# Kernel optimization log

Measured on AMD Instinct MI355X. Metric: run time of the kernel, lower is better.

Reference implementation:

```python
import jax, jax.numpy as jnp
import numpy as np

N = 100000
E = 3200000
NEG_SLOPE = 0.2


def setup_inputs() -> dict:
    key = jax.random.key(0)
    ks = jax.random.split(key, 12)
    x = jax.random.normal(ks[0], (N, 4), dtype=jnp.float32)
    edge_index = jax.random.randint(ks[1], (2, E), 0, N, dtype=jnp.int64)
    # GATConv(4, 16, heads=4): lin (no bias), att_src/att_dst [H, C], bias [H*C]
    W1 = jax.random.normal(ks[2], (4, 4 * 16), dtype=jnp.float32) * 0.5
    as1 = jax.random.normal(ks[3], (4, 16), dtype=jnp.float32) * 0.5
    ad1 = jax.random.normal(ks[4], (4, 16), dtype=jnp.float32) * 0.5
    b1 = jnp.zeros((64,), dtype=jnp.float32)
    # GATConv(64, 2, heads=4)
    W2 = jax.random.normal(ks[5], (64, 4 * 2), dtype=jnp.float32) * 0.125
    as2 = jax.random.normal(ks[6], (4, 2), dtype=jnp.float32) * 0.5
    ad2 = jax.random.normal(ks[7], (4, 2), dtype=jnp.float32) * 0.5
    b2 = jnp.zeros((8,), dtype=jnp.float32)
    # out head Linear(8, 1)
    Wout = jax.random.normal(ks[8], (8, 1), dtype=jnp.float32) * 0.35
    bout = jnp.zeros((1,), dtype=jnp.float32)
    return {"x": x, "edge_index": edge_index, "W1": W1, "as1": as1, "ad1": ad1,
            "b1": b1, "W2": W2, "as2": as2, "ad2": ad2, "b2": b2,
            "Wout": Wout, "bout": bout}


def gat_conv(x, ei, W, a_src, a_dst, b, H, C, n):
    # PyG GATConv (concat=True, negative_slope=0.2), self-loops already in ei
    xw = (x @ W).reshape(n, H, C)                      # [N, H, C]
    src, dst = ei[0], ei[1]
    alpha_s = jnp.einsum('nhc,hc->nh', xw, a_src)      # [N, H]
    alpha_d = jnp.einsum('nhc,hc->nh', xw, a_dst)      # [N, H]
    e = jax.nn.leaky_relu(alpha_s[src] + alpha_d[dst], NEG_SLOPE)  # [E, H]
    # segment softmax over incoming edges of each destination node
    m = jax.ops.segment_max(e, dst, num_segments=n)    # [N, H]
    e = jnp.exp(e - m[dst])
    denom = jax.ops.segment_sum(e, dst, num_segments=n)
    alpha = e / (denom[dst] + 1e-16)                   # [E, H]
    msg = xw[src] * alpha[:, :, None]                  # [E, H, C]
    out = jax.ops.segment_sum(msg, dst, num_segments=n)  # [N, H, C]
    return out.reshape(n, H * C) + b


def reference(x, edge_index, W1, as1, ad1, b1, W2, as2, ad2, b2, Wout, bout):
    n = x.shape[0]
    ar = jnp.arange(n, dtype=edge_index.dtype)
    ei = jnp.concatenate([edge_index, jnp.stack([ar, ar])], axis=1)  # add self-loops
    h = jax.nn.elu(gat_conv(x, ei, W1, as1, ad1, b1, 4, 16, n))       # [N, 64]
    h = jax.nn.elu(gat_conv(h, ei, W2, as2, ad2, b2, 4, 2, n))        # [N, 8]
    g = jnp.mean(h, axis=0, keepdims=True)  # global_mean_pool, batch all zeros -> [1, 8]
    return jax.nn.sigmoid(g @ Wout + bout)  # [1, 1]
```

## Files before the change

### kernel.cpp

```cpp
#include <hip/hip_runtime.h>
#include <hip/hip_fp8.h>

#define NEG 0.2f
#define BSZ 224
#define MAXBUK 512
#define NBIN 512
#define CAP 16384

typedef float v2f __attribute__((ext_vector_type(2)));

__device__ __forceinline__ float elufast(float x){ return x > 0.0f ? x : __expf(x) - 1.0f; }
__device__ __forceinline__ float b2f(unsigned short b){ return __uint_as_float((unsigned)b << 16); }
__device__ __forceinline__ unsigned short f2b(float x){
    unsigned u = __float_as_uint(x);
    return (unsigned short)((u + 0x7FFFu + ((u >> 16) & 1u)) >> 16);
}

__device__ __forceinline__ void fma8(uint2 r, float w, v2f* acc){
    v2f w2 = {w, w};
    v2f f0 = __builtin_amdgcn_cvt_pk_f32_fp8(r.x, false);
    v2f f1 = __builtin_amdgcn_cvt_pk_f32_fp8(r.x, true);
    v2f f2 = __builtin_amdgcn_cvt_pk_f32_fp8(r.y, false);
    v2f f3 = __builtin_amdgcn_cvt_pk_f32_fp8(r.y, true);
    acc[0] = __builtin_elementwise_fma(f0, w2, acc[0]);
    acc[1] = __builtin_elementwise_fma(f1, w2, acc[1]);
    acc[2] = __builtin_elementwise_fma(f2, w2, acc[2]);
    acc[3] = __builtin_elementwise_fma(f3, w2, acc[3]);
}

__global__ void k_l1_node(const float* __restrict__ x, const float* __restrict__ W1,
                          const float* __restrict__ as1, const float* __restrict__ ad1,
                          unsigned char* __restrict__ xw1, uint2* __restrict__ asvb,
                          float* __restrict__ adv, int N){
    __shared__ float sW[256], sA[64], sD[64];
    int tid = threadIdx.x;
    sW[tid] = W1[tid];
    if (tid < 64){ sA[tid] = as1[tid]; sD[tid] = ad1[tid]; }
    __syncthreads();
    int i = blockIdx.x * 256 + tid;
    if (i >= N) return;
    float4 xv = ((const float4*)x)[i];
    const v2f* sW0 = (const v2f*)sW;
    const v2f* sW1v = (const v2f*)(sW + 64);
    const v2f* sW2v = (const v2f*)(sW + 128);
    const v2f* sW3v = (const v2f*)(sW + 192);
    v2f xx = {xv.x, xv.x}, yy = {xv.y, xv.y}, zz = {xv.z, xv.z}, ww = {xv.w, xv.w};
    v2f xwv[32];
    #pragma unroll
    for (int j = 0; j < 32; j++){
        v2f t = xx * sW0[j];
        t = __builtin_elementwise_fma(yy, sW1v[j], t);
        t = __builtin_elementwise_fma(zz, sW2v[j], t);
        t = __builtin_elementwise_fma(ww, sW3v[j], t);
        xwv[j] = t;
    }
    unsigned wv[16];
    #pragma unroll
    for (int j = 0; j < 16; j++){
        unsigned p = 0;
        p = __builtin_amdgcn_cvt_pk_fp8_f32(xwv[2 * j].x,     xwv[2 * j].y,     p, false);
        p = __builtin_amdgcn_cvt_pk_fp8_f32(xwv[2 * j + 1].x, xwv[2 * j + 1].y, p, true);
        wv[j] = p;
    }
    uint4* dp = (uint4*)(xw1 + (size_t)i * 64);
    dp[0] = make_uint4(wv[0],  wv[1],  wv[2],  wv[3]);
    dp[1] = make_uint4(wv[4],  wv[5],  wv[6],  wv[7]);
    dp[2] = make_uint4(wv[8],  wv[9],  wv[10], wv[11]);
    dp[3] = make_uint4(wv[12], wv[13], wv[14], wv[15]);
    const v2f* sAv = (const v2f*)sA;
    const v2f* sDv = (const v2f*)sD;
    float al[4];
    #pragma unroll
    for (int h = 0; h < 4; h++){
        v2f asv = {0.f, 0.f}, adw = {0.f, 0.f};
        #pragma unroll
        for (int c2 = 0; c2 < 8; c2++){
            asv = __builtin_elementwise_fma(xwv[h * 8 + c2], sAv[h * 8 + c2], asv);
            adw = __builtin_elementwise_fma(xwv[h * 8 + c2], sDv[h * 8 + c2], adw);
        }
        al[h] = asv.x + asv.y;
        adv[i * 4 + h] = adw.x + adw.y;
    }
    asvb[i] = make_uint2((unsigned)f2b(al[0]) | ((unsigned)f2b(al[1]) << 16),
                         (unsigned)f2b(al[2]) | ((unsigned)f2b(al[3]) << 16));
}

__global__ void k_bin2(const int* __restrict__ src, const int* __restrict__ dst,
                       int* __restrict__ gcnt, unsigned* __restrict__ staged,
                       int E, int chunksz, int nbuk){
    __shared__ int hist[MAXBUK];
    __shared__ int cur[MAXBUK];
    __shared__ int pend[MAXBUK];
    int tid = threadIdx.x;
    for (int b = tid; b < nbuk; b += 1024) hist[b] = 0;
    __syncthreads();
    int e0 = blockIdx.x * chunksz, e1 = min(E, e0 + chunksz);
    for (int e = e0 + tid; e < e1; e += 1024)
        atomicAdd(&hist[(unsigned)dst[e] / BSZ], 1);
    __syncthreads();
    for (int b = tid; b < nbuk; b += 1024){
        int cnt = hist[b];
        int padded = (cnt + 15) & ~15;
        int base = b * CAP + (padded ? atomicAdd(&gcnt[b], padded) : 0);
        cur[b] = base;
        pend[b] = base + padded;
    }
    __syncthreads();
    for (int e = e0 + tid; e < e1; e += 1024){
        int d = dst[e];
        int buk = (unsigned)d / BSZ;
        int pos = atomicAdd(&cur[buk], 1);
        staged[pos] = (unsigned)src[e] | ((unsigned)(d - buk * BSZ) << 17);
    }
    __syncthreads();
    for (int b = tid; b < nbuk; b += 1024)
        for (int p = cur[b]; p < pend[b]; p++) staged[p] = 0xFFFFFFFFu;
}

__global__ void k_local(const unsigned* __restrict__ staged, const int* __restrict__ gcnt,
                        int2* __restrict__ offp, int* __restrict__ csr, int N){
    __shared__ int deg[BSZ];
    __shared__ int cur[BSZ];
    __shared__ int ts[256];
    int b = blockIdx.x, t = threadIdx.x;
    int lo = b * BSZ, hi = min(N, lo + BSZ);
    int e0 = b * CAP, e1 = e0 + gcnt[b];
    if (t < BSZ) deg[t] = 0;
    __syncthreads();
    for (int e = e0 + t; e < e1; e += 1024){
        unsigned se = staged[e];
        if (se != 0xFFFFFFFFu) atomicAdd(&deg[se >> 17], 1);
    }
    __syncthreads();
    int v = 0;
    if (t < 256){
        v = (t < BSZ) ? deg[t] : 0;
        ts[t] = v;
    }
    __syncthreads();
    for (int s = 1; s < 256; s <<= 1){
        int tmp = (t >= s && t < 256) ? ts[t - s] : 0;
        __syncthreads();
        if (t < 256) ts[t] += tmp;
        __syncthreads();
    }
    if (t < BSZ){
        cur[t] = e0 + ts[t] - v;
        if (lo + t < hi) offp[lo + t] = make_int2(e0 + ts[t] - v, e0 + ts[t]);
    }
    __syncthreads();
    for (int e = e0 + t; e < e1; e += 1024){
        unsigned se = staged[e];
        if (se == 0xFFFFFFFFu) continue;
        int pos = atomicAdd(&cur[se >> 17], 1);
        csr[pos] = (int)(se & 0x1FFFFu);
    }
}

__global__ void k_l1_gather(const int2* __restrict__ offp, const int* __restrict__ csr,
                            const uint2* __restrict__ asvb, const float* __restrict__ adv,
                            const unsigned char* __restrict__ xw1, const float* __restrict__ b1,
                            unsigned char* __restrict__ h1f8, int N){
    int tid = threadIdx.x;
    int wid = (int)(((long)blockIdx.x * 256 + tid) >> 6);
    if (wid >= N) return;
    int lane = tid & 63;
    int g = lane >> 3;
    int q = lane & 7;
    int h = q >> 1;
    float advd = adv[wid * 4 + h];
    const unsigned char* xwq = xw1 + q * 8;
    const char* asvbh = (const char*)asvb + h * 2;

    v2f acc2[4] = {{0.f, 0.f}, {0.f, 0.f}, {0.f, 0.f}, {0.f, 0.f}};
    float den = 0.f;
    int2 rng = offp[wid];
    int k = rng.x, end = rng.y;
    for (; k + 32 <= end; k += 32){
        int s0 = csr[k + g];
        int s1 = csr[k + 8 + g];
        int s2 = csr[k + 16 + g];
        int s3 = csr[k + 24 + g];
        uint2 r0 = *(const uint2*)(xwq + ((size_t)s0 << 6));
        uint2 r1 = *(const uint2*)(xwq + ((size_t)s1 << 6));
        uint2 r2 = *(const uint2*)(xwq + ((size_t)s2 << 6));
        uint2 r3 = *(const uint2*)(xwq + ((size_t)s3 << 6));
        float a0 = b2f(*(const unsigned short*)(asvbh + ((size_t)s0 << 3)));
        float a1 = b2f(*(const unsigned short*)(asvbh + ((size_t)s1 << 3)));
        float a2 = b2f(*(const unsigned short*)(asvbh + ((size_t)s2 << 3)));
        float a3 = b2f(*(const unsigned short*)(asvbh + ((size_t)s3 << 3)));
        float t0 = a0 + advd, t1 = a1 + advd, t2 = a2 + advd, t3 = a3 + advd;
        float w0 = __expf(fmaxf(t0, NEG * t0));
        float w1 = __expf(fmaxf(t1, NEG * t1));
        float w2 = __expf(fmaxf(t2, NEG * t2));
        float w3 = __expf(fmaxf(t3, NEG * t3));
        den += (w0 + w1) + (w2 + w3);
        fma8(r0, w0, acc2);
        fma8(r1, w1, acc2);
        fma8(r2, w2, acc2);
        fma8(r3, w3, acc2);
    }
    if (k + 16 <= end){
        int sA = csr[k + g];
        int sB = csr[k + 8 + g];
        uint2 rA = *(const uint2*)(xwq + ((size_t)sA << 6));
        uint2 rB = *(const uint2*)(xwq + ((size_t)sB << 6));
        float aA = b2f(*(const unsigned short*)(asvbh + ((size_t)sA << 3)));
        float aB = b2f(*(const unsigned short*)(asvbh + ((size_t)sB << 3)));
        float tA = aA + advd, tB = aB + advd;
        float wA = __expf(fmaxf(tA, NEG * tA));
        float wB = __expf(fmaxf(tB, NEG * tB));
        den += wA + wB;
        fma8(rA, wA, acc2);
        fma8(rB, wB, acc2);
        k += 16;
    }
    for (; k < end; k += 8){
        int e = k + g;
        bool valid = e < end;
        int s = csr[valid ? e : end - 1];
        uint2 r = *(const uint2*)(xwq + ((size_t)s << 6));
        float a = b2f(*(const unsigned short*)(asvbh + ((size_t)s << 3)));
        float t = a + advd;
        float w = valid ? __expf(fmaxf(t, NEG * t)) : 0.f;
        den += w;
        fma8(r, w, acc2);
    }

    v2f t0, t1, t2, t3;
    t0.x = __shfl_xor(acc2[0].x, 32); t0.y = __shfl_xor(acc2[0].y, 32);
    t1.x = __shfl_xor(acc2[1].x, 32); t1.y = __shfl_xor(acc2[1].y, 32);
    t2.x = __shfl_xor(acc2[2].x, 32); t2.y = __shfl_xor(acc2[2].y, 32);
    t3.x = __shfl_xor(acc2[3].x, 32); t3.y = __shfl_xor(acc2[3].y, 32);
    bool gb2 = (lane & 32) != 0;
    v2f n0 = gb2 ? (acc2[2] + t2) : (acc2[0] + t0);
    v2f n1 = gb2 ? (acc2[3] + t3) : (acc2[1] + t1);
    v2f u0, u1;
    u0.x = __shfl_xor(n0.x, 16); u0.y = __shfl_xor(n0.y, 16);
    u1.x = __shfl_xor(n1.x, 16); u1.y = __shfl_xor(n1.y, 16);
    bool gb1 = (lane & 16) != 0;
    v2f rr = gb1 ? (n1 + u1) : (n0 + u0);
    v2f z;
    z.x = __shfl_xor(rr.x, 8); z.y = __shfl_xor(rr.y, 8);
    rr += z;
    bool gb0 = (lane & 8) != 0;
    den += __shfl_xor(den, 8);
    den += __shfl_xor(den, 16);
    den += __shfl_xor(den, 32);
    float val = gb0 ? rr.y : rr.x;

    int c = q * 8 + g;
    float aself = b2f(*(const unsigned short*)(asvbh + ((size_t)wid << 3)));
    float tsv = aself + advd;
    float ws = __expf(fmaxf(tsv, NEG * tsv));
    unsigned selfb = xw1[(size_t)wid * 64 + c];
    v2f sf = __builtin_amdgcn_cvt_pk_f32_fp8(selfb, false);
    float asel = val + ws * sf.x;
    float inv = 1.0f / (den + ws + 1e-16f);
    float o = elufast(asel * inv + b1[c]);
    unsigned p = __builtin_amdgcn_cvt_pk_fp8_f32(o, o, 0, false);
    h1f8[(size_t)wid * 64 + c] = (unsigned char)p;
}

__global__ void k_l2_node(const unsigned char* __restrict__ h1f8, const float* __restrict__ W2,
                          const float* __restrict__ ad2, float* __restrict__ xw2,
                          float* __restrict__ adv2, int N){
    __shared__ float sW[512], sD[8];
    int tid = threadIdx.x;
    sW[tid] = W2[tid];
    sW[256 + tid] = W2[256 + tid];
    if (tid < 8) sD[tid] = ad2[tid];
    __syncthreads();
    int i = blockIdx.x * 256 + tid;
    if (i >= N) return;
    const uint2* rp = (const uint2*)(h1f8 + (size_t)i * 64);
    v2f acc2[4] = {{0.f, 0.f}, {0.f, 0.f}, {0.f, 0.f}, {0.f, 0.f}};
    #pragma unroll
    for (int b8 = 0; b8 < 8; b8++){
        uint2 r = rp[b8];
        v2f f0 = __builtin_amdgcn_cvt_pk_f32_fp8(r.x, false);
        v2f f1 = __builtin_amdgcn_cvt_pk_f32_fp8(r.x, true);
        v2f f2 = __builtin_amdgcn_cvt_pk_f32_fp8(r.y, false);
        v2f f3 = __builtin_amdgcn_cvt_pk_f32_fp8(r.y, true);
        float f[8] = {f0.x, f0.y, f1.x, f1.y, f2.x, f2.y, f3.x, f3.y};
        #pragma unroll
        for (int j = 0; j < 8; j++){
            v2f hcv = {f[j], f[j]};
            const v2f* wrow = (const v2f*)&sW[(b8 * 8 + j) * 8];
            acc2[0] = __builtin_elementwise_fma(hcv, wrow[0], acc2[0]);
            acc2[1] = __builtin_elementwise_fma(hcv, wrow[1], acc2[1]);
            acc2[2] = __builtin_elementwise_fma(hcv, wrow[2], acc2[2]);
            acc2[3] = __builtin_elementwise_fma(hcv, wrow[3], acc2[3]);
        }
    }
    float4* xo = (float4*)(xw2 + (size_t)i * 8);
    xo[0] = make_float4(acc2[0].x, acc2[0].y, acc2[1].x, acc2[1].y);
    xo[1] = make_float4(acc2[2].x, acc2[2].y, acc2[3].x, acc2[3].y);
    float4 dv;
    dv.x = acc2[0].x * sD[0] + acc2[0].y * sD[1];
    dv.y = acc2[1].x * sD[2] + acc2[1].y * sD[3];
    dv.z = acc2[2].x * sD[4] + acc2[2].y * sD[5];
    dv.w = acc2[3].x * sD[6] + acc2[3].y * sD[7];
    *(float4*)(adv2 + (size_t)i * 4) = dv;
}

__global__ void k_l2_gather(const int2* __restrict__ offp, const int* __restrict__ csr,
                            const float* __restrict__ adv2, const float* __restrict__ xw2,
                            const float* __restrict__ b2, const float* __restrict__ as2,
                            float* __restrict__ pool, int N){
    __shared__ float lpool[8];
    int tid = threadIdx.x;
    if (tid < 8) lpool[tid] = 0.f;
    __syncthreads();
    int wid = (int)(((long)blockIdx.x * 256 + tid) >> 6);
    if (wid < N){
        int lane = tid & 63;
        int g = lane >> 2;
        int hh = lane & 3;
        float2 a2h = *(const float2*)&as2[hh * 2];
        float advd = adv2[wid * 4 + hh];
        const char* xwh = (const char*)xw2 + hh * 8;
        v2f accv = {0.f, 0.f};
        float den = 0.f;

        auto edge = [&](int s, bool valid){
            v2f v = *(const v2f*)(xwh + ((size_t)s << 5));
            float al = v.x * a2h.x + v.y * a2h.y;
            float t = al + advd;
            float w = valid ? __expf(fmaxf(t, NEG * t)) : 0.f;
            den += w;
            v2f w2 = {w, w};
            accv = __builtin_elementwise_fma(v, w2, accv);
        };

        int2 rng = offp[wid];
        int k = rng.x, end = rng.y;
        for (; k + 32 <= end; k += 32){
            int s0 = csr[k + g], s1 = csr[k + 16 + g];
            edge(s0, true); edge(s1, true);
        }
        for (; k < end; k += 16){
            int e = k + g;
            bool valid = e < end;
            int s = csr[valid ? e : end - 1];
            edge(s, valid);
        }
        #pragma unroll
        for (int m = 4; m <= 32; m <<= 1){
            accv.x += __shfl_xor(accv.x, m);
            accv.y += __shfl_xor(accv.y, m);
            den    += __shfl_xor(den, m);
        }
        if (g == 0){
            v2f v = *(const v2f*)(xwh + ((size_t)wid << 5));
            float al = v.x * a2h.x + v.y * a2h.y;
            float t = al + advd;
            float ws = __expf(fmaxf(t, NEG * t));
            den += ws;
            accv.x += ws * v.x;
            accv.y += ws * v.y;
            float inv = 1.0f / (den + 1e-16f);
            float o0 = elufast(accv.x * inv + b2[hh * 2]);
            float o1 = elufast(accv.y * inv + b2[hh * 2 + 1]);
            atomicAdd(&lpool[hh * 2], o0);
            atomicAdd(&lpool[hh * 2 + 1], o1);
        }
    }
    __syncthreads();
    if (tid < 8) atomicAdd(&pool[(blockIdx.x & 63) * 8 + tid], lpool[tid]);
}

__global__ void k_final(const float* __restrict__ pool, const float* __restrict__ Wout,
                        const float* __restrict__ bout, float* __restrict__ out, float invN){
    int lane = threadIdx.x;
    const float4* p4 = (const float4*)(pool + lane * 8);
    float4 a = p4[0], b = p4[1];
    float v[8] = {a.x, a.y, a.z, a.w, b.x, b.y, b.z, b.w};
    #pragma unroll
    for (int m = 1; m <= 32; m <<= 1){
        #pragma unroll
        for (int j = 0; j < 8; j++) v[j] += __shfl_xor(v[j], m);
    }
    if (lane == 0){
        float z = bout[0];
        #pragma unroll
        for (int j = 0; j < 8; j++) z += v[j] * invN * Wout[j];
        out[0] = 1.0f / (1.0f + __expf(-z));
    }
}

extern "C" void kernel_launch(void* const* d_in, const int* in_sizes, int n_in,
                              void* d_out, int out_size, void* d_ws, size_t ws_size,
                              hipStream_t stream){
    const float* x    = (const float*)d_in[0];
    const int*   ei   = (const int*)d_in[1];
    const float* W1   = (const float*)d_in[2];
    const float* as1  = (const float*)d_in[3];
    const float* ad1  = (const float*)d_in[4];
    const float* b1   = (const float*)d_in[5];
    const float* W2   = (const float*)d_in[6];
    const float* as2  = (const float*)d_in[7];
    const float* ad2  = (const float*)d_in[8];
    const float* b2   = (const float*)d_in[9];
    const float* Wout = (const float*)d_in[10];
    const float* bout = (const float*)d_in[11];
    float* out = (float*)d_out;

    int N = in_sizes[0] / 4;
    int E = in_sizes[1] / 2;
    const int* src = ei;
    const int* dst = ei + E;

    char* ws = (char*)d_ws;
    size_t off_b = 0;
    auto alloc = [&](size_t bytes)->void*{
        void* p = ws + off_b;
        off_b += (bytes + 255) & ~(size_t)255;
        return p;
    };
    unsigned char* xw1  = (unsigned char*)alloc((size_t)N * 64);
    unsigned char* h1f8 = (unsigned char*)alloc((size_t)N * 64);
    uint2*    asvb   = (uint2*)alloc((size_t)N * 8);
    float*    adv    = (float*)alloc((size_t)N * 4 * 4);
    float*    adv2   = (float*)alloc((size_t)N * 4 * 4);
    int*      gcnt   = (int*)alloc((size_t)MAXBUK * 4);
    unsigned* staged = (unsigned*)alloc((size_t)MAXBUK * CAP * 4);
    int2*     offp   = (int2*)alloc((size_t)N * 8);
    int*      csr    = (int*)alloc((size_t)MAXBUK * CAP * 4);
    float*    xw2    = (float*)alloc((size_t)N * 8 * 4);
    float*    pool   = (float*)alloc(64 * 8 * 4);

    int nbuk = (N + BSZ - 1) / BSZ;
    int chunksz = (E + NBIN - 1) / NBIN;

    hipMemsetAsync(pool, 0, 64 * 8 * 4, stream);
    hipMemsetAsync(gcnt, 0, (size_t)MAXBUK * 4, stream);

    k_bin2<<<NBIN, 1024, 0, stream>>>(src, dst, gcnt, staged, E, chunksz, nbuk);
    k_l1_node<<<(N + 255) / 256, 256, 0, stream>>>(x, W1, as1, ad1, xw1, asvb, adv, N);
    k_local<<<nbuk, 1024, 0, stream>>>(staged, gcnt, offp, csr, N);

    k_l1_gather<<<(int)(((long)N * 64 + 255) / 256), 256, 0, stream>>>(
        offp, csr, asvb, adv, xw1, b1, h1f8, N);
    k_l2_node<<<(N + 255) / 256, 256, 0, stream>>>(h1f8, W2, ad2, xw2, adv2, N);
    k_l2_gather<<<(int)(((long)N * 64 + 255) / 256), 256, 0, stream>>>(
        offp, csr, adv2, xw2, b2, as2, pool, N);
    k_final<<<1, 64, 0, stream>>>(pool, Wout, bout, out, 1.0f / (float)N);
}
```

Before: 177.3 us.

## Stage binned edges in LDS and write buckets contiguously to global memory

The binning kernel now computes a local prefix sum over bucket histograms, scatters packed edges into a shared-memory staging buffer, then has each wavefront copy whole buckets to global memory with coalesced writes, padding included. This replaces scattered per-edge global stores and the serial per-thread padding loop. It needs a large LDS allocation (about 25KB plus scan arrays), which may reduce occupancy, and it assumes each chunk holds at most LSTG edges.

```diff
diff --git a/kernel.cpp b/kernel.cpp
--- a/kernel.cpp
+++ b/kernel.cpp
@@ -6,6 +6,7 @@
 #define MAXBUK 512
 #define NBIN 512
 #define CAP 16384
+#define LSTG 6400
 
 typedef float v2f __attribute__((ext_vector_type(2)));
 
@@ -90,31 +91,49 @@
                        int E, int chunksz, int nbuk){
     __shared__ int hist[MAXBUK];
     __shared__ int cur[MAXBUK];
-    __shared__ int pend[MAXBUK];
+    __shared__ int lsb[MAXBUK];
+    __shared__ int gbase[MAXBUK];
+    __shared__ int ts[512];
+    __shared__ unsigned lstg[LSTG];
     int tid = threadIdx.x;
-    for (int b = tid; b < nbuk; b += 1024) hist[b] = 0;
+    for (int b = tid; b < MAXBUK; b += 1024) hist[b] = 0;
     __syncthreads();
     int e0 = blockIdx.x * chunksz, e1 = min(E, e0 + chunksz);
     for (int e = e0 + tid; e < e1; e += 1024)
         atomicAdd(&hist[(unsigned)dst[e] / BSZ], 1);
     __syncthreads();
-    for (int b = tid; b < nbuk; b += 1024){
-        int cnt = hist[b];
-        int padded = (cnt + 15) & ~15;
-        int base = b * CAP + (padded ? atomicAdd(&gcnt[b], padded) : 0);
-        cur[b] = base;
-        pend[b] = base + padded;
+    int v = 0;
+    if (tid < 512){ v = hist[tid]; ts[tid] = v; }
+    __syncthreads();
+    for (int s = 1; s < 512; s <<= 1){
+        int tmp = (tid >= s && tid < 512) ? ts[tid - s] : 0;
+        __syncthreads();
+        if (tid < 512) ts[tid] += tmp;
+        __syncthreads();
+    }
+    if (tid < 512){
+        int excl = ts[tid] - v;
+        lsb[tid] = excl;
+        cur[tid] = excl;
+        int padded = (v + 15) & ~15;
+        gbase[tid] = tid * CAP + (padded ? atomicAdd(&gcnt[tid], padded) : 0);
     }
     __syncthreads();
     for (int e = e0 + tid; e < e1; e += 1024){
         int d = dst[e];
         int buk = (unsigned)d / BSZ;
         int pos = atomicAdd(&cur[buk], 1);
-        staged[pos] = (unsigned)src[e] | ((unsigned)(d - buk * BSZ) << 17);
-    }
-    __syncthreads();
-    for (int b = tid; b < nbuk; b += 1024)
-        for (int p = cur[b]; p < pend[b]; p++) staged[p] = 0xFFFFFFFFu;
+        lstg[pos] = (unsigned)src[e] | ((unsigned)(d - buk * BSZ) << 17);
+    }
+    __syncthreads();
+    int wv = tid >> 6, ln = tid & 63;
+    for (int b = wv; b < nbuk; b += 16){
+        int cnt = hist[b];
+        int padded = (cnt + 15) & ~15;
+        int lb = lsb[b], gb = gbase[b];
+        for (int j = ln; j < padded; j += 64)
+            staged[gb + j] = (j < cnt) ? lstg[lb + j] : 0xFFFFFFFFu;
+    }
 }
 
 __global__ void k_local(const unsigned* __restrict__ staged, const int* __restrict__ gcnt,
```

Result: faster. 168.4 us (-5.0%).
